# Optimization experiments

Hardware: AMD Instinct MI355X
Metric: run time of the kernel (lower is better)

Reference implementation:

```python
import jax, jax.numpy as jnp
import numpy as np

TOP_K = 2


def setup_inputs() -> dict:
    key = jax.random.key(0)
    ks = jax.random.split(key, 5)
    B, S, D, E, I = 1, 2048, 2880, 8, 2880
    scale_in = 1.0 / np.sqrt(D)
    scale_mid = 1.0 / np.sqrt(I)
    return {
        "x": jax.random.normal(ks[0], (B, S, D), dtype=jnp.float32),
        "w_router": jax.random.normal(ks[1], (D, E), dtype=jnp.float32) * scale_in,
        "w_gate": jax.random.normal(ks[2], (E, D, I), dtype=jnp.float32) * scale_in,
        "w_up": jax.random.normal(ks[3], (E, D, I), dtype=jnp.float32) * scale_in,
        "w_down": jax.random.normal(ks[4], (E, I, D), dtype=jnp.float32) * scale_mid,
    }


def reference(x, w_router, w_gate, w_up, w_down):
    B, S, D = x.shape
    E = w_router.shape[1]
    t = x.reshape(-1, D)  # [T, D] flattened tokens

    # --- RouterTopK: softmax over experts, then top-k selection ---
    logits = t @ w_router                      # [T, E]
    affinities = jax.nn.softmax(logits, axis=-1)
    top_vals, top_idx = jax.lax.top_k(affinities, TOP_K)   # [T, K]
    # normalize_top_k_affinities=True: renormalize selected weights to sum to 1
    top_vals = top_vals / jnp.sum(top_vals, axis=-1, keepdims=True)

    # scatter normalized weights into dense [T, E] combine matrix
    T = t.shape[0]
    tok = jnp.arange(T)[:, None]
    weights = jnp.zeros((T, E), dtype=t.dtype).at[tok, top_idx].set(top_vals)

    # --- Expert SiLU-GLU MLPs (computed per expert, combined by weights) ---
    gate = jnp.einsum("td,edi->eti", t, w_gate)  # [E, T, I]
    up = jnp.einsum("td,edi->eti", t, w_up)      # [E, T, I]
    h = jax.nn.silu(gate) * up                   # [E, T, I]
    y = jnp.einsum("eti,eid->etd", h, w_down)    # [E, T, D]

    out = jnp.einsum("te,etd->td", weights, y)   # affinity-weighted combine
    return out.reshape(B, S, D)
```

## Files before the change

kernel.cpp:

```cpp
#include <hip/hip_runtime.h>
#include <hip/hip_fp16.h>
#include <stdint.h>
#include <math.h>


typedef _Float16 f16;
typedef _Float16 f16x8 __attribute__((ext_vector_type(8)));
typedef float f32x4 __attribute__((ext_vector_type(4)));

#define T_TOK 2048
#define DDIM 2880
#define NEXP 8
#define IDIM 2880

#define BM 256
#define BK 64
#define NKT 45
#define BN1 96
#define NNT1 30
#define BN2 192
#define NNT2 15
#define MAXMT 24
#define NB1 (NNT1*MAXMT)
#define NB2 (NNT2*MAXMT)
#define SLOT_CAP 6144

#define HBUF_OFF 0
#define HBUF_BYTES ((size_t)SLOT_CAP*IDIM*2)
#define XH_OFF   (HBUF_OFF + HBUF_BYTES)
#define XH_BYTES ((size_t)T_TOK*DDIM*2)
#define YBUF_OFF XH_OFF
#define YBUF_BYTES ((size_t)SLOT_CAP*DDIM*2)
#define META_OFF (YBUF_OFF + YBUF_BYTES)
#define M_COUNT 0
#define M_CUR 8
#define M_OFFS 16
#define M_NTILES 25
#define M_TILE_E 32
#define M_TILE_R0 96
#define M_SLOT_TOK 160
#define M_SLOT_OF (160+SLOT_CAP)
#define M_TOK_E (M_SLOT_OF + 2*T_TOK)
#define META_INTS (M_TOK_E + 2*T_TOK)
#define SLOTW_OFF (META_OFF + META_INTS*4)
#define TOKW_OFF  (SLOTW_OFF + SLOT_CAP*4)
#define WS_NEEDED ((size_t)TOKW_OFF + (size_t)T_TOK*2*4)

__device__ __forceinline__ int swz(int row) { return ((row ^ (row >> 3)) & 7) << 4; }

__device__ __forceinline__ void gload_lds16(const void* gp, void* lp) {
  __builtin_amdgcn_global_load_lds(
      (const __attribute__((address_space(1))) uint32_t*)gp,
      (__attribute__((address_space(3))) uint32_t*)lp,
      16, 0, 0);
}

__global__ __launch_bounds__(256) void k_router(
    const float* __restrict__ x, const float* __restrict__ wr,
    int* __restrict__ meta, float* __restrict__ tok_w) {
  const int lane = threadIdx.x & 63;
  const int t = blockIdx.x * 4 + (threadIdx.x >> 6);
  double acc[NEXP];
#pragma unroll
  for (int e = 0; e < NEXP; e++) acc[e] = 0.0;
  for (int d = lane; d < DDIM; d += 64) {
    float xv = x[(size_t)t * DDIM + d];
    float4 w0 = *(const float4*)(wr + (size_t)d * NEXP);
    float4 w1 = *(const float4*)(wr + (size_t)d * NEXP + 4);
    acc[0] += (double)xv * (double)w0.x;
    acc[1] += (double)xv * (double)w0.y;
    acc[2] += (double)xv * (double)w0.z;
    acc[3] += (double)xv * (double)w0.w;
    acc[4] += (double)xv * (double)w1.x;
    acc[5] += (double)xv * (double)w1.y;
    acc[6] += (double)xv * (double)w1.z;
    acc[7] += (double)xv * (double)w1.w;
  }
#pragma unroll
  for (int m = 32; m >= 1; m >>= 1) {
#pragma unroll
    for (int e = 0; e < NEXP; e++) acc[e] += __shfl_xor(acc[e], m, 64);
  }
  if (lane == 0) {
    int e0 = 0;
#pragma unroll
    for (int e = 1; e < NEXP; e++) if (acc[e] > acc[e0]) e0 = e;
    int e1 = (e0 == 0) ? 1 : 0;
#pragma unroll
    for (int e = 0; e < NEXP; e++) if (e != e0 && acc[e] > acc[e1]) e1 = e;
    double w0 = 1.0 / (1.0 + exp(acc[e1] - acc[e0]));
    meta[M_TOK_E + 2*t]     = e0;
    meta[M_TOK_E + 2*t + 1] = e1;
    tok_w[2*t]     = (float)w0;
    tok_w[2*t + 1] = (float)(1.0 - w0);
    atomicAdd(&meta[M_COUNT + e0], 1);
    atomicAdd(&meta[M_COUNT + e1], 1);
  }
}

__global__ __launch_bounds__(256) void k_xcvt(const float* __restrict__ x, f16* __restrict__ xh) {
  size_t i = ((size_t)blockIdx.x * 256 + threadIdx.x) * 8;
  float4 a = *(const float4*)(x + i);
  float4 b = *(const float4*)(x + i + 4);
  f16x8 v;
  v[0]=(f16)a.x; v[1]=(f16)a.y; v[2]=(f16)a.z; v[3]=(f16)a.w;
  v[4]=(f16)b.x; v[5]=(f16)b.y; v[6]=(f16)b.z; v[7]=(f16)b.w;
  *(f16x8*)(xh + i) = v;
}

__global__ __launch_bounds__(64) void k_scan(int* __restrict__ meta, float* __restrict__ slot_w) {
  __shared__ int s_off[NEXP], s_cnt[NEXP], s_pc[NEXP];
  if (threadIdx.x == 0) {
    int run = 0, nt = 0;
    for (int e = 0; e < NEXP; e++) {
      int c = meta[M_COUNT + e];
      int mt = (c + BM - 1) / BM;
      meta[M_OFFS + e] = run;
      s_off[e] = run; s_cnt[e] = c; s_pc[e] = mt * BM;
      for (int j = 0; j < mt; j++) { meta[M_TILE_E + nt] = e; meta[M_TILE_R0 + nt] = run + j * BM; nt++; }
      run += mt * BM;
      meta[M_CUR + e] = 0;
    }
    meta[M_OFFS + NEXP] = run;
    meta[M_NTILES] = nt;
  }
  __syncthreads();
  for (int e = 0; e < NEXP; e++) {
    for (int i = s_cnt[e] + (int)threadIdx.x; i < s_pc[e]; i += 64) {
      meta[M_SLOT_TOK + s_off[e] + i] = 0;
      slot_w[s_off[e] + i] = 0.0f;
    }
  }
}

__global__ __launch_bounds__(256) void k_scatter(int* __restrict__ meta,
    float* __restrict__ slot_w, const float* __restrict__ tok_w) {
  int t = blockIdx.x * 256 + threadIdx.x;
  if (t >= T_TOK) return;
#pragma unroll
  for (int k = 0; k < 2; k++) {
    int e = meta[M_TOK_E + 2*t + k];
    int pos = atomicAdd(&meta[M_CUR + e], 1);
    int slot = meta[M_OFFS + e] + pos;
    meta[M_SLOT_TOK + slot] = t;
    slot_w[slot] = tok_w[2*t + k];
    meta[M_SLOT_OF + 2*t + k] = slot;
  }
}

__global__ __launch_bounds__(512, 2) void k_gemm1(
    const f16* __restrict__ xh, const float* __restrict__ wg, const float* __restrict__ wu,
    f16* __restrict__ hbuf, const int* __restrict__ meta) {
  const int id = blockIdx.x;
  const int sid = (id & 7) * (NB1 / 8) + (id >> 3);
  const int mt = sid % MAXMT;
  const int nb = sid / MAXMT;
  if (mt >= meta[M_NTILES]) return;
  const int e  = meta[M_TILE_E + mt];
  const int r0 = meta[M_TILE_R0 + mt];
  const int n0 = nb * BN1;

  __shared__ ushort sA[2][BM * BK];
  __shared__ ushort sB[2][2][BN1 * BK];

  const int tid  = threadIdx.x;
  const int lane = tid & 63;
  const int w    = tid >> 6;
  const int wm   = w >> 1;
  const int gu   = w & 1;

  const char* a_gbase[4];
  int a_loff[4];
#pragma unroll
  for (int i = 0; i < 4; i++) {
    int seg = w * 4 + i;
    int row = seg * 8 + (lane >> 3);
    int colb = ((lane & 7) * 16) ^ swz(row);
    int tok = meta[M_SLOT_TOK + r0 + row];
    a_gbase[i] = (const char*)(xh + (size_t)tok * DDIM) + colb;
    a_loff[i] = seg * 1024;
  }

  const int bm_ = tid / 192;
  const int tt  = tid % 192;
  const int bn0 = (tt % 24) * 4;
  const int bk0 = (tt / 24) * 8;
  const bool bact = tid < 384;
  const float* bsrc = (bm_ ? wu : wg) + ((size_t)e * DDIM + bk0) * IDIM + n0 + bn0;

  float4 vB[8];
  f32x4 acc[4][6];
#pragma unroll
  for (int i = 0; i < 4; i++)
#pragma unroll
    for (int j = 0; j < 6; j++) acc[i][j] = {0.f,0.f,0.f,0.f};

#pragma unroll
  for (int i = 0; i < 4; i++) gload_lds16(a_gbase[i], (char*)sA[0] + a_loff[i]);
  if (bact) {
#pragma unroll
    for (int j = 0; j < 8; j++) vB[j] = *(const float4*)(bsrc + (size_t)j * IDIM);
#pragma unroll
    for (int c = 0; c < 4; c++) {
      f16x8 p;
#pragma unroll
      for (int j = 0; j < 8; j++) {
        float fc = (c==0) ? vB[j].x : (c==1) ? vB[j].y : (c==2) ? vB[j].z : vB[j].w;
        p[j] = (f16)fc;
      }
      *(f16x8*)((char*)sB[0][bm_] + (bn0 + c) * 128 + ((bk0 * 2) ^ swz(bn0 + c))) = p;
    }
  }
  __syncthreads();

  for (int kt = 0; kt < NKT; kt++) {
    const int cur = kt & 1;
    if (kt + 1 < NKT) {
#pragma unroll
      for (int i = 0; i < 4; i++)
        gload_lds16(a_gbase[i] + (kt + 1) * 128, (char*)sA[cur ^ 1] + a_loff[i]);
      if (bact) {
        const float* bs = bsrc + (size_t)(kt + 1) * BK * IDIM;
#pragma unroll
        for (int j = 0; j < 8; j++) vB[j] = *(const float4*)(bs + (size_t)j * IDIM);
      }
    }
#pragma unroll
    for (int kk = 0; kk < 2; kk++) {
      const int gb = kk * 64 + ((lane >> 4) * 16);
      f16x8 af[4], bf[6];
#pragma unroll
      for (int fm = 0; fm < 4; fm++) {
        int row = wm * 64 + fm * 16 + (lane & 15);
        af[fm] = *(const f16x8*)((const char*)sA[cur] + row * 128 + (gb ^ swz(row)));
      }
#pragma unroll
      for (int fn = 0; fn < 6; fn++) {
        int row = fn * 16 + (lane & 15);
        bf[fn] = *(const f16x8*)((const char*)sB[cur][gu] + row * 128 + (gb ^ swz(row)));
      }
#pragma unroll
      for (int fm = 0; fm < 4; fm++)
#pragma unroll
        for (int fn = 0; fn < 6; fn++)
          acc[fm][fn] = __builtin_amdgcn_mfma_f32_16x16x32_f16(af[fm], bf[fn], acc[fm][fn], 0, 0, 0);
    }
    if (kt + 1 < NKT && bact) {
#pragma unroll
      for (int c = 0; c < 4; c++) {
        f16x8 p;
#pragma unroll
        for (int j = 0; j < 8; j++) {
          float fc = (c==0) ? vB[j].x : (c==1) ? vB[j].y : (c==2) ? vB[j].z : vB[j].w;
          p[j] = (f16)fc;
        }
        *(f16x8*)((char*)sB[cur ^ 1][bm_] + (bn0 + c) * 128 + ((bk0 * 2) ^ swz(bn0 + c))) = p;
      }
    }
    __syncthreads();
  }

  float* u_lds = (float*)&sA[0][0];
  const int rl4 = (lane >> 4) * 4;
  const int cl  = lane & 15;
#pragma unroll
  for (int r = 0; r < 2; r++) {
    __syncthreads();
    if (gu == 1) {
#pragma unroll
      for (int fi = 0; fi < 2; fi++)
#pragma unroll
        for (int fn = 0; fn < 6; fn++)
#pragma unroll
          for (int j = 0; j < 4; j++)
            u_lds[wm * 3200 + (fi * 16 + rl4 + j) * 100 + fn * 16 + cl] = acc[2*r + fi][fn][j];
    }
    __syncthreads();
    if (gu == 0) {
#pragma unroll
      for (int fi = 0; fi < 2; fi++) {
        int fm = 2*r + fi;
#pragma unroll
        for (int fn = 0; fn < 6; fn++)
#pragma unroll
          for (int j = 0; j < 4; j++) {
            float u = u_lds[wm * 3200 + (fi * 16 + rl4 + j) * 100 + fn * 16 + cl];
            float g = acc[fm][fn][j];
            float h = g * u / (1.0f + __expf(-g));
            hbuf[(size_t)(r0 + wm * 64 + fm * 16 + rl4 + j) * IDIM + n0 + fn * 16 + cl] = (f16)h;
          }
      }
    }
  }
}

__global__ __launch_bounds__(512, 2) void k_gemm2(
    const f16* __restrict__ hbuf, const float* __restrict__ wd,
    f16* __restrict__ ybuf, const int* __restrict__ meta, const float* __restrict__ slot_w) {
  const int id = blockIdx.x;
  const int sid = (id & 7) * (NB2 / 8) + (id >> 3);
  const int mt = sid % MAXMT;
  const int nb = sid / MAXMT;
  if (mt >= meta[M_NTILES]) return;
  const int e  = meta[M_TILE_E + mt];
  const int r0 = meta[M_TILE_R0 + mt];
  const int n0 = nb * BN2;

  __shared__ ushort sA[2][BM * BK];
  __shared__ ushort sB1[2][BN2 * BK];

  const int tid  = threadIdx.x;
  const int lane = tid & 63;
  const int w    = tid >> 6;
  const int wm   = w >> 1;
  const int wn   = w & 1;

  const char* a_gbase[4];
  int a_loff[4];
#pragma unroll
  for (int i = 0; i < 4; i++) {
    int seg = w * 4 + i;
    int row = seg * 8 + (lane >> 3);
    int colb = ((lane & 7) * 16) ^ swz(row);
    a_gbase[i] = (const char*)(hbuf + (size_t)(r0 + row) * IDIM) + colb;
    a_loff[i] = seg * 1024;
  }

  const int half = tid / 192;
  const int tt   = tid % 192;
  const int bn0  = half * 96 + (tt % 24) * 4;
  const int bk0  = (tt / 24) * 8;
  const bool bact = tid < 384;
  const float* bsrc = wd + ((size_t)e * IDIM + bk0) * DDIM + n0 + bn0;

  float4 vB[8];
  f32x4 acc[4][6];
#pragma unroll
  for (int i = 0; i < 4; i++)
#pragma unroll
    for (int j = 0; j < 6; j++) acc[i][j] = {0.f,0.f,0.f,0.f};

#pragma unroll
  for (int i = 0; i < 4; i++) gload_lds16(a_gbase[i], (char*)sA[0] + a_loff[i]);
  if (bact) {
#pragma unroll
    for (int j = 0; j < 8; j++) vB[j] = *(const float4*)(bsrc + (size_t)j * DDIM);
#pragma unroll
    for (int c = 0; c < 4; c++) {
      f16x8 p;
#pragma unroll
      for (int j = 0; j < 8; j++) {
        float fc = (c==0) ? vB[j].x : (c==1) ? vB[j].y : (c==2) ? vB[j].z : vB[j].w;
        p[j] = (f16)fc;
      }
      *(f16x8*)((char*)sB1[0] + (bn0 + c) * 128 + ((bk0 * 2) ^ swz(bn0 + c))) = p;
    }
  }
  __syncthreads();

  for (int kt = 0; kt < NKT; kt++) {
    const int cur = kt & 1;
    if (kt + 1 < NKT) {
#pragma unroll
      for (int i = 0; i < 4; i++)
        gload_lds16(a_gbase[i] + (kt + 1) * 128, (char*)sA[cur ^ 1] + a_loff[i]);
      if (bact) {
        const float* bs = bsrc + (size_t)(kt + 1) * BK * DDIM;
#pragma unroll
        for (int j = 0; j < 8; j++) vB[j] = *(const float4*)(bs + (size_t)j * DDIM);
      }
    }
#pragma unroll
    for (int kk = 0; kk < 2; kk++) {
      const int gb = kk * 64 + ((lane >> 4) * 16);
      f16x8 af[4], bf[6];
#pragma unroll
      for (int fm = 0; fm < 4; fm++) {
        int row = wm * 64 + fm * 16 + (lane & 15);
        af[fm] = *(const f16x8*)((const char*)sA[cur] + row * 128 + (gb ^ swz(row)));
      }
#pragma unroll
      for (int fn = 0; fn < 6; fn++) {
        int row = wn * 96 + fn * 16 + (lane & 15);
        bf[fn] = *(const f16x8*)((const char*)sB1[cur] + row * 128 + (gb ^ swz(row)));
      }
#pragma unroll
      for (int fm = 0; fm < 4; fm++)
#pragma unroll
        for (int fn = 0; fn < 6; fn++)
          acc[fm][fn] = __builtin_amdgcn_mfma_f32_16x16x32_f16(af[fm], bf[fn], acc[fm][fn], 0, 0, 0);
    }
    if (kt + 1 < NKT && bact) {
#pragma unroll
      for (int c = 0; c < 4; c++) {
        f16x8 p;
#pragma unroll
        for (int j = 0; j < 8; j++) {
          float fc = (c==0) ? vB[j].x : (c==1) ? vB[j].y : (c==2) ? vB[j].z : vB[j].w;
          p[j] = (f16)fc;
        }
        *(f16x8*)((char*)sB1[cur ^ 1] + (bn0 + c) * 128 + ((bk0 * 2) ^ swz(bn0 + c))) = p;
      }
    }
    __syncthreads();
  }

  const int rl4 = (lane >> 4) * 4;
  const int cl  = lane & 15;
#pragma unroll
  for (int fm = 0; fm < 4; fm++)
#pragma unroll
    for (int j = 0; j < 4; j++) {
      int row = wm * 64 + fm * 16 + rl4 + j;
      int slot = r0 + row;
      float wv = slot_w[slot];
#pragma unroll
      for (int fn = 0; fn < 6; fn++) {
        int col = n0 + wn * 96 + fn * 16 + cl;
        ybuf[(size_t)slot * DDIM + col] = (f16)(acc[fm][fn][j] * wv);
      }
    }
}

__global__ __launch_bounds__(256) void k_combine(const f16* __restrict__ ybuf,
    const int* __restrict__ meta, float* __restrict__ out) {
  size_t idx = (size_t)blockIdx.x * 256 + threadIdx.x;
  int t = (int)(idx / (DDIM/8));
  int c = (int)(idx % (DDIM/8));
  int s0 = meta[M_SLOT_OF + 2*t];
  int s1 = meta[M_SLOT_OF + 2*t + 1];
  f16x8 a = *(const f16x8*)(ybuf + (size_t)s0 * DDIM + c*8);
  f16x8 b = *(const f16x8*)(ybuf + (size_t)s1 * DDIM + c*8);
  float4 o0, o1;
  o0.x = (float)a[0] + (float)b[0];
  o0.y = (float)a[1] + (float)b[1];
  o0.z = (float)a[2] + (float)b[2];
  o0.w = (float)a[3] + (float)b[3];
  o1.x = (float)a[4] + (float)b[4];
  o1.y = (float)a[5] + (float)b[5];
  o1.z = (float)a[6] + (float)b[6];
  o1.w = (float)a[7] + (float)b[7];
  float* op = out + (size_t)t * DDIM + c*8;
  *(float4*)op = o0;
  *(float4*)(op + 4) = o1;
}

extern "C" void kernel_launch(void* const* d_in, const int* in_sizes, int n_in,
                              void* d_out, int out_size, void* d_ws, size_t ws_size,
                              hipStream_t stream) {
  const float* x  = (const float*)d_in[0];
  const float* wr = (const float*)d_in[1];
  const float* wg = (const float*)d_in[2];
  const float* wu = (const float*)d_in[3];
  const float* wd = (const float*)d_in[4];
  float* out = (float*)d_out;
  char* ws = (char*)d_ws;
  if (ws_size < WS_NEEDED) return;

  f16* hbuf  = (f16*)(ws + HBUF_OFF);
  f16* xh    = (f16*)(ws + XH_OFF);
  f16* ybuf  = (f16*)(ws + YBUF_OFF);
  int* meta  = (int*)(ws + META_OFF);
  float* slot_w = (float*)(ws + SLOTW_OFF);
  float* tok_w  = (float*)(ws + TOKW_OFF);

  hipMemsetAsync(meta + M_COUNT, 0, NEXP * sizeof(int), stream);
  k_router<<<T_TOK/4, 256, 0, stream>>>(x, wr, meta, tok_w);
  k_xcvt<<<(T_TOK*DDIM/8 + 255)/256, 256, 0, stream>>>(x, xh);
  k_scan<<<1, 64, 0, stream>>>(meta, slot_w);
  k_scatter<<<(T_TOK + 255)/256, 256, 0, stream>>>(meta, slot_w, tok_w);
  k_gemm1<<<NB1, 512, 0, stream>>>(xh, wg, wu, hbuf, meta);
  k_gemm2<<<NB2, 512, 0, stream>>>(hbuf, wd, ybuf, meta, slot_w);
  k_combine<<<(T_TOK*DDIM/8 + 255)/256, 256, 0, stream>>>(ybuf, meta, out);
}
```

Baseline: 687.3 us.

## Pre-convert expert weights to transposed fp16 and stream via direct LDS loads

Adds a kernel that converts the gate, up and down weights on every call from fp32 into a transposed fp16 layout in workspace. Both expert GEMMs can then load weight tiles straight into LDS with global_load_lds, instead of loading fp32 into registers and converting inside the K loop. The GEMMs also move to 128-row tiles with 256 threads, and the up and gate products now share the A fragments in one kernel. In exchange the new path pays a full weight read-convert-write pass each call, needs a much larger workspace, and drops the double-buffered K pipeline. The old kernels stay as a fallback for when the workspace is too small.

```diff
diff --git a/kernel.cpp b/kernel.cpp
--- a/kernel.cpp
+++ b/kernel.cpp
@@ -12,26 +12,24 @@
 #define DDIM 2880
 #define NEXP 8
 #define IDIM 2880
-
-#define BM 256
 #define BK 64
 #define NKT 45
-#define BN1 96
-#define NNT1 30
-#define BN2 192
-#define NNT2 15
-#define MAXMT 24
-#define NB1 (NNT1*MAXMT)
-#define NB2 (NNT2*MAXMT)
+
+#define BM_A 128
+#define BN1_A 96
+#define BN2_A 192
+#define MAXMT_A 40
+#define NB1_A (30*MAXMT_A)
+#define NB2_A (15*MAXMT_A)
+#define BM_B 256
+#define BN1_B 96
+#define BN2_B 192
+#define MAXMT_B 24
+#define NB1_B (30*MAXMT_B)
+#define NB2_B (15*MAXMT_B)
+
 #define SLOT_CAP 6144
 
-#define HBUF_OFF 0
-#define HBUF_BYTES ((size_t)SLOT_CAP*IDIM*2)
-#define XH_OFF   (HBUF_OFF + HBUF_BYTES)
-#define XH_BYTES ((size_t)T_TOK*DDIM*2)
-#define YBUF_OFF XH_OFF
-#define YBUF_BYTES ((size_t)SLOT_CAP*DDIM*2)
-#define META_OFF (YBUF_OFF + YBUF_BYTES)
 #define M_COUNT 0
 #define M_CUR 8
 #define M_OFFS 16
@@ -42,9 +40,26 @@
 #define M_SLOT_OF (160+SLOT_CAP)
 #define M_TOK_E (M_SLOT_OF + 2*T_TOK)
 #define META_INTS (M_TOK_E + 2*T_TOK)
-#define SLOTW_OFF (META_OFF + META_INTS*4)
-#define TOKW_OFF  (SLOTW_OFF + SLOT_CAP*4)
-#define WS_NEEDED ((size_t)TOKW_OFF + (size_t)T_TOK*2*4)
+
+#define WT_B   ((size_t)NEXP*DDIM*IDIM*2)
+#define A_WGT  ((size_t)0)
+#define A_WUT  (A_WGT + WT_B)
+#define A_WDT  A_WGT
+#define A_HBUF (A_WUT + WT_B)
+#define A_YBUF (A_HBUF + (size_t)5120*IDIM*2)
+#define A_XH   (A_YBUF + (size_t)5120*DDIM*2)
+#define A_META (A_XH + (size_t)T_TOK*DDIM*2)
+#define A_SLOTW (A_META + (size_t)META_INTS*4)
+#define A_TOKW  (A_SLOTW + (size_t)SLOT_CAP*4)
+#define A_NEED  (A_TOKW + (size_t)T_TOK*2*4)
+
+#define B_HBUF ((size_t)0)
+#define B_XH   (B_HBUF + (size_t)SLOT_CAP*IDIM*2)
+#define B_YBUF B_XH
+#define B_META (B_YBUF + (size_t)SLOT_CAP*DDIM*2)
+#define B_SLOTW (B_META + (size_t)META_INTS*4)
+#define B_TOKW  (B_SLOTW + (size_t)SLOT_CAP*4)
+#define B_NEED  (B_TOKW + (size_t)T_TOK*2*4)
 
 __device__ __forceinline__ int swz(int row) { return ((row ^ (row >> 3)) & 7) << 4; }
 
@@ -108,17 +123,45 @@
   *(f16x8*)(xh + i) = v;
 }
 
-__global__ __launch_bounds__(64) void k_scan(int* __restrict__ meta, float* __restrict__ slot_w) {
+__global__ __launch_bounds__(256) void k_cvt_w(const float* __restrict__ src, f16* __restrict__ dst) {
+  __shared__ f16 t[64][72];
+  const int tile = blockIdx.x;
+  const int e = blockIdx.y;
+  const int k0 = (tile / 45) * 64;
+  const int i0 = (tile % 45) * 64;
+  const int tid = threadIdx.x;
+  const float* sp = src + ((size_t)e * DDIM + k0) * IDIM + i0;
+#pragma unroll
+  for (int p = 0; p < 4; p++) {
+    int kr = p * 16 + (tid >> 4);
+    int c0 = (tid & 15) * 4;
+    float4 v = *(const float4*)(sp + (size_t)kr * IDIM + c0);
+    t[c0 + 0][kr] = (f16)v.x;
+    t[c0 + 1][kr] = (f16)v.y;
+    t[c0 + 2][kr] = (f16)v.z;
+    t[c0 + 3][kr] = (f16)v.w;
+  }
+  __syncthreads();
+#pragma unroll
+  for (int p = 0; p < 2; p++) {
+    int row = tid >> 2;
+    int ch = (tid & 3) + p * 4;
+    f16x8 o = *(const f16x8*)&t[row][ch * 8];
+    *(f16x8*)(dst + ((size_t)e * IDIM + i0 + row) * DDIM + k0 + ch * 8) = o;
+  }
+}
+
+__global__ __launch_bounds__(64) void k_scan(int* __restrict__ meta, float* __restrict__ slot_w, int bm) {
   __shared__ int s_off[NEXP], s_cnt[NEXP], s_pc[NEXP];
   if (threadIdx.x == 0) {
     int run = 0, nt = 0;
     for (int e = 0; e < NEXP; e++) {
       int c = meta[M_COUNT + e];
-      int mt = (c + BM - 1) / BM;
+      int mt = (c + bm - 1) / bm;
       meta[M_OFFS + e] = run;
-      s_off[e] = run; s_cnt[e] = c; s_pc[e] = mt * BM;
-      for (int j = 0; j < mt; j++) { meta[M_TILE_E + nt] = e; meta[M_TILE_R0 + nt] = run + j * BM; nt++; }
-      run += mt * BM;
+      s_off[e] = run; s_cnt[e] = c; s_pc[e] = mt * bm;
+      for (int j = 0; j < mt; j++) { meta[M_TILE_E + nt] = e; meta[M_TILE_R0 + nt] = run + j * bm; nt++; }
+      run += mt * bm;
       meta[M_CUR + e] = 0;
     }
     meta[M_OFFS + NEXP] = run;
@@ -148,228 +191,156 @@
   }
 }
 
-__global__ __launch_bounds__(512, 2) void k_gemm1(
-    const f16* __restrict__ xh, const float* __restrict__ wg, const float* __restrict__ wu,
+
+__global__ __launch_bounds__(256, 3) void kg1(
+    const f16* __restrict__ xh, const f16* __restrict__ wgT, const f16* __restrict__ wuT,
     f16* __restrict__ hbuf, const int* __restrict__ meta) {
   const int id = blockIdx.x;
-  const int sid = (id & 7) * (NB1 / 8) + (id >> 3);
-  const int mt = sid % MAXMT;
-  const int nb = sid / MAXMT;
+  const int sid = (id & 7) * (NB1_A / 8) + (id >> 3);
+  const int mt = sid % MAXMT_A;
+  const int nb = sid / MAXMT_A;
   if (mt >= meta[M_NTILES]) return;
   const int e  = meta[M_TILE_E + mt];
   const int r0 = meta[M_TILE_R0 + mt];
-  const int n0 = nb * BN1;
-
-  __shared__ ushort sA[2][BM * BK];
-  __shared__ ushort sB[2][2][BN1 * BK];
-
-  const int tid  = threadIdx.x;
+  const int n0 = nb * BN1_A;
+
+  __shared__ ushort sA[BM_A * BK];
+  __shared__ ushort sBg[BN1_A * BK];
+  __shared__ ushort sBu[BN1_A * BK];
+
+  const int tid = threadIdx.x;
   const int lane = tid & 63;
-  const int w    = tid >> 6;
-  const int wm   = w >> 1;
-  const int gu   = w & 1;
-
-  const char* a_gbase[4];
-  int a_loff[4];
+  const int w = tid >> 6;
+  const int wm = w >> 1, wn = w & 1;
+
+  const char* aG[4]; int aL[4];
 #pragma unroll
   for (int i = 0; i < 4; i++) {
     int seg = w * 4 + i;
     int row = seg * 8 + (lane >> 3);
     int colb = ((lane & 7) * 16) ^ swz(row);
     int tok = meta[M_SLOT_TOK + r0 + row];
-    a_gbase[i] = (const char*)(xh + (size_t)tok * DDIM) + colb;
-    a_loff[i] = seg * 1024;
-  }
-
-  const int bm_ = tid / 192;
-  const int tt  = tid % 192;
-  const int bn0 = (tt % 24) * 4;
-  const int bk0 = (tt / 24) * 8;
-  const bool bact = tid < 384;
-  const float* bsrc = (bm_ ? wu : wg) + ((size_t)e * DDIM + bk0) * IDIM + n0 + bn0;
-
-  float4 vB[8];
-  f32x4 acc[4][6];
+    aG[i] = (const char*)(xh + (size_t)tok * DDIM) + colb;
+    aL[i] = seg * 1024;
+  }
+  const char* gG[3]; const char* uG[3]; int bL[3];
+#pragma unroll
+  for (int i = 0; i < 3; i++) {
+    int seg = w * 3 + i;
+    int row = seg * 8 + (lane >> 3);
+    int colb = ((lane & 7) * 16) ^ swz(row);
+    gG[i] = (const char*)(wgT + ((size_t)e * IDIM + n0 + row) * DDIM) + colb;
+    uG[i] = (const char*)(wuT + ((size_t)e * IDIM + n0 + row) * DDIM) + colb;
+    bL[i] = seg * 1024;
+  }
+
+  f32x4 accG[4][3], accU[4][3];
 #pragma unroll
   for (int i = 0; i < 4; i++)
 #pragma unroll
-    for (int j = 0; j < 6; j++) acc[i][j] = {0.f,0.f,0.f,0.f};
-
-#pragma unroll
-  for (int i = 0; i < 4; i++) gload_lds16(a_gbase[i], (char*)sA[0] + a_loff[i]);
-  if (bact) {
-#pragma unroll
-    for (int j = 0; j < 8; j++) vB[j] = *(const float4*)(bsrc + (size_t)j * IDIM);
-#pragma unroll
-    for (int c = 0; c < 4; c++) {
-      f16x8 p;
-#pragma unroll
-      for (int j = 0; j < 8; j++) {
-        float fc = (c==0) ? vB[j].x : (c==1) ? vB[j].y : (c==2) ? vB[j].z : vB[j].w;
-        p[j] = (f16)fc;
-      }
-      *(f16x8*)((char*)sB[0][bm_] + (bn0 + c) * 128 + ((bk0 * 2) ^ swz(bn0 + c))) = p;
-    }
-  }
-  __syncthreads();
+    for (int j = 0; j < 3; j++) { accG[i][j] = {0.f,0.f,0.f,0.f}; accU[i][j] = {0.f,0.f,0.f,0.f}; }
 
   for (int kt = 0; kt < NKT; kt++) {
-    const int cur = kt & 1;
-    if (kt + 1 < NKT) {
-#pragma unroll
-      for (int i = 0; i < 4; i++)
-        gload_lds16(a_gbase[i] + (kt + 1) * 128, (char*)sA[cur ^ 1] + a_loff[i]);
-      if (bact) {
-        const float* bs = bsrc + (size_t)(kt + 1) * BK * IDIM;
-#pragma unroll
-        for (int j = 0; j < 8; j++) vB[j] = *(const float4*)(bs + (size_t)j * IDIM);
-      }
-    }
+    __syncthreads();
+#pragma unroll
+    for (int i = 0; i < 4; i++) gload_lds16(aG[i] + kt * 128, (char*)sA + aL[i]);
+#pragma unroll
+    for (int i = 0; i < 3; i++) gload_lds16(gG[i] + kt * 128, (char*)sBg + bL[i]);
+#pragma unroll
+    for (int i = 0; i < 3; i++) gload_lds16(uG[i] + kt * 128, (char*)sBu + bL[i]);
+    __syncthreads();
 #pragma unroll
     for (int kk = 0; kk < 2; kk++) {
       const int gb = kk * 64 + ((lane >> 4) * 16);
-      f16x8 af[4], bf[6];
+      f16x8 af[4], bg[3], bu[3];
 #pragma unroll
       for (int fm = 0; fm < 4; fm++) {
         int row = wm * 64 + fm * 16 + (lane & 15);
-        af[fm] = *(const f16x8*)((const char*)sA[cur] + row * 128 + (gb ^ swz(row)));
-      }
-#pragma unroll
-      for (int fn = 0; fn < 6; fn++) {
-        int row = fn * 16 + (lane & 15);
-        bf[fn] = *(const f16x8*)((const char*)sB[cur][gu] + row * 128 + (gb ^ swz(row)));
+        af[fm] = *(const f16x8*)((const char*)sA + row * 128 + (gb ^ swz(row)));
+      }
+#pragma unroll
+      for (int fn = 0; fn < 3; fn++) {
+        int row = wn * 48 + fn * 16 + (lane & 15);
+        bg[fn] = *(const f16x8*)((const char*)sBg + row * 128 + (gb ^ swz(row)));
+        bu[fn] = *(const f16x8*)((const char*)sBu + row * 128 + (gb ^ swz(row)));
       }
 #pragma unroll
       for (int fm = 0; fm < 4; fm++)
 #pragma unroll
-        for (int fn = 0; fn < 6; fn++)
-          acc[fm][fn] = __builtin_amdgcn_mfma_f32_16x16x32_f16(af[fm], bf[fn], acc[fm][fn], 0, 0, 0);
-    }
-    if (kt + 1 < NKT && bact) {
-#pragma unroll
-      for (int c = 0; c < 4; c++) {
-        f16x8 p;
-#pragma unroll
-        for (int j = 0; j < 8; j++) {
-          float fc = (c==0) ? vB[j].x : (c==1) ? vB[j].y : (c==2) ? vB[j].z : vB[j].w;
-          p[j] = (f16)fc;
+        for (int fn = 0; fn < 3; fn++) {
+          accG[fm][fn] = __builtin_amdgcn_mfma_f32_16x16x32_f16(af[fm], bg[fn], accG[fm][fn], 0, 0, 0);
+          accU[fm][fn] = __builtin_amdgcn_mfma_f32_16x16x32_f16(af[fm], bu[fn], accU[fm][fn], 0, 0, 0);
         }
-        *(f16x8*)((char*)sB[cur ^ 1][bm_] + (bn0 + c) * 128 + ((bk0 * 2) ^ swz(bn0 + c))) = p;
-      }
-    }
-    __syncthreads();
-  }
-
-  float* u_lds = (float*)&sA[0][0];
+    }
+  }
   const int rl4 = (lane >> 4) * 4;
   const int cl  = lane & 15;
 #pragma unroll
-  for (int r = 0; r < 2; r++) {
-    __syncthreads();
-    if (gu == 1) {
-#pragma unroll
-      for (int fi = 0; fi < 2; fi++)
-#pragma unroll
-        for (int fn = 0; fn < 6; fn++)
-#pragma unroll
-          for (int j = 0; j < 4; j++)
-            u_lds[wm * 3200 + (fi * 16 + rl4 + j) * 100 + fn * 16 + cl] = acc[2*r + fi][fn][j];
-    }
-    __syncthreads();
-    if (gu == 0) {
-#pragma unroll
-      for (int fi = 0; fi < 2; fi++) {
-        int fm = 2*r + fi;
-#pragma unroll
-        for (int fn = 0; fn < 6; fn++)
-#pragma unroll
-          for (int j = 0; j < 4; j++) {
-            float u = u_lds[wm * 3200 + (fi * 16 + rl4 + j) * 100 + fn * 16 + cl];
-            float g = acc[fm][fn][j];
-            float h = g * u / (1.0f + __expf(-g));
-            hbuf[(size_t)(r0 + wm * 64 + fm * 16 + rl4 + j) * IDIM + n0 + fn * 16 + cl] = (f16)h;
-          }
-      }
-    }
-  }
-}
-
-__global__ __launch_bounds__(512, 2) void k_gemm2(
-    const f16* __restrict__ hbuf, const float* __restrict__ wd,
+  for (int fm = 0; fm < 4; fm++)
+#pragma unroll
+    for (int fn = 0; fn < 3; fn++)
+#pragma unroll
+      for (int j = 0; j < 4; j++) {
+        int row = wm * 64 + fm * 16 + rl4 + j;
+        int col = n0 + wn * 48 + fn * 16 + cl;
+        float g = accG[fm][fn][j], u = accU[fm][fn][j];
+        float h = g * u / (1.0f + __expf(-g));
+        hbuf[(size_t)(r0 + row) * IDIM + col] = (f16)h;
+      }
+}
+
+__global__ __launch_bounds__(256, 3) void kg2(
+    const f16* __restrict__ hbuf, const f16* __restrict__ wdT,
     f16* __restrict__ ybuf, const int* __restrict__ meta, const float* __restrict__ slot_w) {
   const int id = blockIdx.x;
-  const int sid = (id & 7) * (NB2 / 8) + (id >> 3);
-  const int mt = sid % MAXMT;
-  const int nb = sid / MAXMT;
+  const int sid = (id & 7) * (NB2_A / 8) + (id >> 3);
+  const int mt = sid % MAXMT_A;
+  const int nb = sid / MAXMT_A;
   if (mt >= meta[M_NTILES]) return;
   const int e  = meta[M_TILE_E + mt];
   const int r0 = meta[M_TILE_R0 + mt];
-  const int n0 = nb * BN2;
-
-  __shared__ ushort sA[2][BM * BK];
-  __shared__ ushort sB1[2][BN2 * BK];
-
-  const int tid  = threadIdx.x;
+  const int n0 = nb * BN2_A;
+
+  __shared__ ushort sA[BM_A * BK];
+  __shared__ ushort sB[BN2_A * BK];
+
+  const int tid = threadIdx.x;
   const int lane = tid & 63;
-  const int w    = tid >> 6;
-  const int wm   = w >> 1;
-  const int wn   = w & 1;
-
-  const char* a_gbase[4];
-  int a_loff[4];
+  const int w = tid >> 6;
+  const int wm = w >> 1, wn = w & 1;
+
+  const char* aG[4]; int aL[4];
 #pragma unroll
   for (int i = 0; i < 4; i++) {
     int seg = w * 4 + i;
     int row = seg * 8 + (lane >> 3);
     int colb = ((lane & 7) * 16) ^ swz(row);
-    a_gbase[i] = (const char*)(hbuf + (size_t)(r0 + row) * IDIM) + colb;
-    a_loff[i] = seg * 1024;
-  }
-
-  const int half = tid / 192;
-  const int tt   = tid % 192;
-  const int bn0  = half * 96 + (tt % 24) * 4;
-  const int bk0  = (tt / 24) * 8;
-  const bool bact = tid < 384;
-  const float* bsrc = wd + ((size_t)e * IDIM + bk0) * DDIM + n0 + bn0;
-
-  float4 vB[8];
+    aG[i] = (const char*)(hbuf + (size_t)(r0 + row) * IDIM) + colb;
+    aL[i] = seg * 1024;
+  }
+  const char* bG[6]; int bL[6];
+#pragma unroll
+  for (int i = 0; i < 6; i++) {
+    int seg = w * 6 + i;
+    int row = seg * 8 + (lane >> 3);
+    int colb = ((lane & 7) * 16) ^ swz(row);
+    bG[i] = (const char*)(wdT + ((size_t)e * DDIM + n0 + row) * IDIM) + colb;
+    bL[i] = seg * 1024;
+  }
+
   f32x4 acc[4][6];
 #pragma unroll
   for (int i = 0; i < 4; i++)
 #pragma unroll
     for (int j = 0; j < 6; j++) acc[i][j] = {0.f,0.f,0.f,0.f};
 
-#pragma unroll
-  for (int i = 0; i < 4; i++) gload_lds16(a_gbase[i], (char*)sA[0] + a_loff[i]);
-  if (bact) {
-#pragma unroll
-    for (int j = 0; j < 8; j++) vB[j] = *(const float4*)(bsrc + (size_t)j * DDIM);
-#pragma unroll
-    for (int c = 0; c < 4; c++) {
-      f16x8 p;
-#pragma unroll
-      for (int j = 0; j < 8; j++) {
-        float fc = (c==0) ? vB[j].x : (c==1) ? vB[j].y : (c==2) ? vB[j].z : vB[j].w;
-        p[j] = (f16)fc;
-      }
-      *(f16x8*)((char*)sB1[0] + (bn0 + c) * 128 + ((bk0 * 2) ^ swz(bn0 + c))) = p;
-    }
-  }
-  __syncthreads();
-
   for (int kt = 0; kt < NKT; kt++) {
-    const int cur = kt & 1;
-    if (kt + 1 < NKT) {
-#pragma unroll
-      for (int i = 0; i < 4; i++)
-        gload_lds16(a_gbase[i] + (kt + 1) * 128, (char*)sA[cur ^ 1] + a_loff[i]);
-      if (bact) {
-        const float* bs = bsrc + (size_t)(kt + 1) * BK * DDIM;
-#pragma unroll
-        for (int j = 0; j < 8; j++) vB[j] = *(const float4*)(bs + (size_t)j * DDIM);
-      }
-    }
+    __syncthreads();
+#pragma unroll
+    for (int i = 0; i < 4; i++) gload_lds16(aG[i] + kt * 128, (char*)sA + aL[i]);
+#pragma unroll
+    for (int i = 0; i < 6; i++) gload_lds16(bG[i] + kt * 128, (char*)sB + bL[i]);
+    __syncthreads();
 #pragma unroll
     for (int kk = 0; kk < 2; kk++) {
       const int gb = kk * 64 + ((lane >> 4) * 16);
@@ -377,12 +348,12 @@
 #pragma unroll
       for (int fm = 0; fm < 4; fm++) {
         int row = wm * 64 + fm * 16 + (lane & 15);
-        af[fm] = *(const f16x8*)((const char*)sA[cur] + row * 128 + (gb ^ swz(row)));
+        af[fm] = *(const f16x8*)((const char*)sA + row * 128 + (gb ^ swz(row)));
       }
 #pragma unroll
       for (int fn = 0; fn < 6; fn++) {
         int row = wn * 96 + fn * 16 + (lane & 15);
-        bf[fn] = *(const f16x8*)((const char*)sB1[cur] + row * 128 + (gb ^ swz(row)));
+        bf[fn] = *(const f16x8*)((const char*)sB + row * 128 + (gb ^ swz(row)));
       }
 #pragma unroll
       for (int fm = 0; fm < 4; fm++)
@@ -390,21 +361,7 @@
         for (int fn = 0; fn < 6; fn++)
           acc[fm][fn] = __builtin_amdgcn_mfma_f32_16x16x32_f16(af[fm], bf[fn], acc[fm][fn], 0, 0, 0);
     }
-    if (kt + 1 < NKT && bact) {
-#pragma unroll
-      for (int c = 0; c < 4; c++) {
-        f16x8 p;
-#pragma unroll
-        for (int j = 0; j < 8; j++) {
-          float fc = (c==0) ? vB[j].x : (c==1) ? vB[j].y : (c==2) ? vB[j].z : vB[j].w;
-          p[j] = (f16)fc;
-        }
-        *(f16x8*)((char*)sB1[cur ^ 1] + (bn0 + c) * 128 + ((bk0 * 2) ^ swz(bn0 + c))) = p;
-      }
-    }
-    __syncthreads();
-  }
-
+  }
   const int rl4 = (lane >> 4) * 4;
   const int cl  = lane & 15;
 #pragma unroll
@@ -445,6 +402,279 @@
   *(float4*)(op + 4) = o1;
 }
 
+
+__global__ __launch_bounds__(512, 2) void kg1_fb(
+    const f16* __restrict__ xh, const float* __restrict__ wg, const float* __restrict__ wu,
+    f16* __restrict__ hbuf, const int* __restrict__ meta) {
+  const int id = blockIdx.x;
+  const int sid = (id & 7) * (NB1_B / 8) + (id >> 3);
+  const int mt = sid % MAXMT_B;
+  const int nb = sid / MAXMT_B;
+  if (mt >= meta[M_NTILES]) return;
+  const int e  = meta[M_TILE_E + mt];
+  const int r0 = meta[M_TILE_R0 + mt];
+  const int n0 = nb * BN1_B;
+
+  __shared__ ushort sA[2][BM_B * BK];
+  __shared__ ushort sB[2][2][BN1_B * BK];
+
+  const int tid  = threadIdx.x;
+  const int lane = tid & 63;
+  const int w    = tid >> 6;
+  const int wm   = w >> 1;
+  const int gu   = w & 1;
+
+  const char* a_gbase[4];
+  int a_loff[4];
+#pragma unroll
+  for (int i = 0; i < 4; i++) {
+    int seg = w * 4 + i;
+    int row = seg * 8 + (lane >> 3);
+    int colb = ((lane & 7) * 16) ^ swz(row);
+    int tok = meta[M_SLOT_TOK + r0 + row];
+    a_gbase[i] = (const char*)(xh + (size_t)tok * DDIM) + colb;
+    a_loff[i] = seg * 1024;
+  }
+  const int bm_ = tid / 192;
+  const int tt  = tid % 192;
+  const int bn0 = (tt % 24) * 4;
+  const int bk0 = (tt / 24) * 8;
+  const bool bact = tid < 384;
+  const float* bsrc = (bm_ ? wu : wg) + ((size_t)e * DDIM + bk0) * IDIM + n0 + bn0;
+
+  float4 vB[8];
+  f32x4 acc[4][6];
+#pragma unroll
+  for (int i = 0; i < 4; i++)
+#pragma unroll
+    for (int j = 0; j < 6; j++) acc[i][j] = {0.f,0.f,0.f,0.f};
+
+#pragma unroll
+  for (int i = 0; i < 4; i++) gload_lds16(a_gbase[i], (char*)sA[0] + a_loff[i]);
+  if (bact) {
+#pragma unroll
+    for (int j = 0; j < 8; j++) vB[j] = *(const float4*)(bsrc + (size_t)j * IDIM);
+#pragma unroll
+    for (int c = 0; c < 4; c++) {
+      f16x8 p;
+#pragma unroll
+      for (int j = 0; j < 8; j++) {
+        float fc = (c==0) ? vB[j].x : (c==1) ? vB[j].y : (c==2) ? vB[j].z : vB[j].w;
+        p[j] = (f16)fc;
+      }
+      *(f16x8*)((char*)sB[0][bm_] + (bn0 + c) * 128 + ((bk0 * 2) ^ swz(bn0 + c))) = p;
+    }
+  }
+  __syncthreads();
+
+  for (int kt = 0; kt < NKT; kt++) {
+    const int cur = kt & 1;
+    if (kt + 1 < NKT) {
+#pragma unroll
+      for (int i = 0; i < 4; i++)
+        gload_lds16(a_gbase[i] + (kt + 1) * 128, (char*)sA[cur ^ 1] + a_loff[i]);
+      if (bact) {
+        const float* bs = bsrc + (size_t)(kt + 1) * BK * IDIM;
+#pragma unroll
+        for (int j = 0; j < 8; j++) vB[j] = *(const float4*)(bs + (size_t)j * IDIM);
+      }
+    }
+#pragma unroll
+    for (int kk = 0; kk < 2; kk++) {
+      const int gb = kk * 64 + ((lane >> 4) * 16);
+      f16x8 af[4], bf[6];
+#pragma unroll
+      for (int fm = 0; fm < 4; fm++) {
+        int row = wm * 64 + fm * 16 + (lane & 15);
+        af[fm] = *(const f16x8*)((const char*)sA[cur] + row * 128 + (gb ^ swz(row)));
+      }
+#pragma unroll
+      for (int fn = 0; fn < 6; fn++) {
+        int row = fn * 16 + (lane & 15);
+        bf[fn] = *(const f16x8*)((const char*)sB[cur][gu] + row * 128 + (gb ^ swz(row)));
+      }
+#pragma unroll
+      for (int fm = 0; fm < 4; fm++)
+#pragma unroll
+        for (int fn = 0; fn < 6; fn++)
+          acc[fm][fn] = __builtin_amdgcn_mfma_f32_16x16x32_f16(af[fm], bf[fn], acc[fm][fn], 0, 0, 0);
+    }
+    if (kt + 1 < NKT && bact) {
+#pragma unroll
+      for (int c = 0; c < 4; c++) {
+        f16x8 p;
+#pragma unroll
+        for (int j = 0; j < 8; j++) {
+          float fc = (c==0) ? vB[j].x : (c==1) ? vB[j].y : (c==2) ? vB[j].z : vB[j].w;
+          p[j] = (f16)fc;
+        }
+        *(f16x8*)((char*)sB[cur ^ 1][bm_] + (bn0 + c) * 128 + ((bk0 * 2) ^ swz(bn0 + c))) = p;
+      }
+    }
+    __syncthreads();
+  }
+
+  float* u_lds = (float*)&sA[0][0];
+  const int rl4 = (lane >> 4) * 4;
+  const int cl  = lane & 15;
+#pragma unroll
+  for (int r = 0; r < 2; r++) {
+    __syncthreads();
+    if (gu == 1) {
+#pragma unroll
+      for (int fi = 0; fi < 2; fi++)
+#pragma unroll
+        for (int fn = 0; fn < 6; fn++)
+#pragma unroll
+          for (int j = 0; j < 4; j++)
+            u_lds[wm * 3200 + (fi * 16 + rl4 + j) * 100 + fn * 16 + cl] = acc[2*r + fi][fn][j];
+    }
+    __syncthreads();
+    if (gu == 0) {
+#pragma unroll
+      for (int fi = 0; fi < 2; fi++) {
+        int fm = 2*r + fi;
+#pragma unroll
+        for (int fn = 0; fn < 6; fn++)
+#pragma unroll
+          for (int j = 0; j < 4; j++) {
+            float u = u_lds[wm * 3200 + (fi * 16 + rl4 + j) * 100 + fn * 16 + cl];
+            float g = acc[fm][fn][j];
+            float h = g * u / (1.0f + __expf(-g));
+            hbuf[(size_t)(r0 + wm * 64 + fm * 16 + rl4 + j) * IDIM + n0 + fn * 16 + cl] = (f16)h;
+          }
+      }
+    }
+  }
+}
+
+__global__ __launch_bounds__(512, 2) void kg2_fb(
+    const f16* __restrict__ hbuf, const float* __restrict__ wd,
+    f16* __restrict__ ybuf, const int* __restrict__ meta, const float* __restrict__ slot_w) {
+  const int id = blockIdx.x;
+  const int sid = (id & 7) * (NB2_B / 8) + (id >> 3);
+  const int mt = sid % MAXMT_B;
+  const int nb = sid / MAXMT_B;
+  if (mt >= meta[M_NTILES]) return;
+  const int e  = meta[M_TILE_E + mt];
+  const int r0 = meta[M_TILE_R0 + mt];
+  const int n0 = nb * BN2_B;
+
+  __shared__ ushort sA[2][BM_B * BK];
+  __shared__ ushort sB1[2][BN2_B * BK];
+
+  const int tid  = threadIdx.x;
+  const int lane = tid & 63;
+  const int w    = tid >> 6;
+  const int wm   = w >> 1;
+  const int wn   = w & 1;
+
+  const char* a_gbase[4];
+  int a_loff[4];
+#pragma unroll
+  for (int i = 0; i < 4; i++) {
+    int seg = w * 4 + i;
+    int row = seg * 8 + (lane >> 3);
+    int colb = ((lane & 7) * 16) ^ swz(row);
+    a_gbase[i] = (const char*)(hbuf + (size_t)(r0 + row) * IDIM) + colb;
+    a_loff[i] = seg * 1024;
+  }
+  const int half = tid / 192;
+  const int tt   = tid % 192;
+  const int bn0  = half * 96 + (tt % 24) * 4;
+  const int bk0  = (tt / 24) * 8;
+  const bool bact = tid < 384;
+  const float* bsrc = wd + ((size_t)e * IDIM + bk0) * DDIM + n0 + bn0;
+
+  float4 vB[8];
+  f32x4 acc[4][6];
+#pragma unroll
+  for (int i = 0; i < 4; i++)
+#pragma unroll
+    for (int j = 0; j < 6; j++) acc[i][j] = {0.f,0.f,0.f,0.f};
+
+#pragma unroll
+  for (int i = 0; i < 4; i++) gload_lds16(a_gbase[i], (char*)sA[0] + a_loff[i]);
+  if (bact) {
+#pragma unroll
+    for (int j = 0; j < 8; j++) vB[j] = *(const float4*)(bsrc + (size_t)j * DDIM);
+#pragma unroll
+    for (int c = 0; c < 4; c++) {
+      f16x8 p;
+#pragma unroll
+      for (int j = 0; j < 8; j++) {
+        float fc = (c==0) ? vB[j].x : (c==1) ? vB[j].y : (c==2) ? vB[j].z : vB[j].w;
+        p[j] = (f16)fc;
+      }
+      *(f16x8*)((char*)sB1[0] + (bn0 + c) * 128 + ((bk0 * 2) ^ swz(bn0 + c))) = p;
+    }
+  }
+  __syncthreads();
+
+  for (int kt = 0; kt < NKT; kt++) {
+    const int cur = kt & 1;
+    if (kt + 1 < NKT) {
+#pragma unroll
+      for (int i = 0; i < 4; i++)
+        gload_lds16(a_gbase[i] + (kt + 1) * 128, (char*)sA[cur ^ 1] + a_loff[i]);
+      if (bact) {
+        const float* bs = bsrc + (size_t)(kt + 1) * BK * DDIM;
+#pragma unroll
+        for (int j = 0; j < 8; j++) vB[j] = *(const float4*)(bs + (size_t)j * DDIM);
+      }
+    }
+#pragma unroll
+    for (int kk = 0; kk < 2; kk++) {
+      const int gb = kk * 64 + ((lane >> 4) * 16);
+      f16x8 af[4], bf[6];
+#pragma unroll
+      for (int fm = 0; fm < 4; fm++) {
+        int row = wm * 64 + fm * 16 + (lane & 15);
+        af[fm] = *(const f16x8*)((const char*)sA[cur] + row * 128 + (gb ^ swz(row)));
+      }
+#pragma unroll
+      for (int fn = 0; fn < 6; fn++) {
+        int row = wn * 96 + fn * 16 + (lane & 15);
+        bf[fn] = *(const f16x8*)((const char*)sB1[cur] + row * 128 + (gb ^ swz(row)));
+      }
+#pragma unroll
+      for (int fm = 0; fm < 4; fm++)
+#pragma unroll
+        for (int fn = 0; fn < 6; fn++)
+          acc[fm][fn] = __builtin_amdgcn_mfma_f32_16x16x32_f16(af[fm], bf[fn], acc[fm][fn], 0, 0, 0);
+    }
+    if (kt + 1 < NKT && bact) {
+#pragma unroll
+      for (int c = 0; c < 4; c++) {
+        f16x8 p;
+#pragma unroll
+        for (int j = 0; j < 8; j++) {
+          float fc = (c==0) ? vB[j].x : (c==1) ? vB[j].y : (c==2) ? vB[j].z : vB[j].w;
+          p[j] = (f16)fc;
+        }
+        *(f16x8*)((char*)sB1[cur ^ 1] + (bn0 + c) * 128 + ((bk0 * 2) ^ swz(bn0 + c))) = p;
+      }
+    }
+    __syncthreads();
+  }
+
+  const int rl4 = (lane >> 4) * 4;
+  const int cl  = lane & 15;
+#pragma unroll
+  for (int fm = 0; fm < 4; fm++)
+#pragma unroll
+    for (int j = 0; j < 4; j++) {
+      int row = wm * 64 + fm * 16 + rl4 + j;
+      int slot = r0 + row;
+      float wv = slot_w[slot];
+#pragma unroll
+      for (int fn = 0; fn < 6; fn++) {
+        int col = n0 + wn * 96 + fn * 16 + cl;
+        ybuf[(size_t)slot * DDIM + col] = (f16)(acc[fm][fn][j] * wv);
+      }
+    }
+}
+
 extern "C" void kernel_launch(void* const* d_in, const int* in_sizes, int n_in,
                               void* d_out, int out_size, void* d_ws, size_t ws_size,
                               hipStream_t stream) {
@@ -455,21 +685,44 @@
   const float* wd = (const float*)d_in[4];
   float* out = (float*)d_out;
   char* ws = (char*)d_ws;
-  if (ws_size < WS_NEEDED) return;
-
-  f16* hbuf  = (f16*)(ws + HBUF_OFF);
-  f16* xh    = (f16*)(ws + XH_OFF);
-  f16* ybuf  = (f16*)(ws + YBUF_OFF);
-  int* meta  = (int*)(ws + META_OFF);
-  float* slot_w = (float*)(ws + SLOTW_OFF);
-  float* tok_w  = (float*)(ws + TOKW_OFF);
-
-  hipMemsetAsync(meta + M_COUNT, 0, NEXP * sizeof(int), stream);
-  k_router<<<T_TOK/4, 256, 0, stream>>>(x, wr, meta, tok_w);
-  k_xcvt<<<(T_TOK*DDIM/8 + 255)/256, 256, 0, stream>>>(x, xh);
-  k_scan<<<1, 64, 0, stream>>>(meta, slot_w);
-  k_scatter<<<(T_TOK + 255)/256, 256, 0, stream>>>(meta, slot_w, tok_w);
-  k_gemm1<<<NB1, 512, 0, stream>>>(xh, wg, wu, hbuf, meta);
-  k_gemm2<<<NB2, 512, 0, stream>>>(hbuf, wd, ybuf, meta, slot_w);
-  k_combine<<<(T_TOK*DDIM/8 + 255)/256, 256, 0, stream>>>(ybuf, meta, out);
-}
+
+  if (ws_size >= A_NEED) {
+    f16* wgT = (f16*)(ws + A_WGT);
+    f16* wuT = (f16*)(ws + A_WUT);
+    f16* wdT = (f16*)(ws + A_WDT);
+    f16* hbuf = (f16*)(ws + A_HBUF);
+    f16* ybuf = (f16*)(ws + A_YBUF);
+    f16* xh   = (f16*)(ws + A_XH);
+    int* meta = (int*)(ws + A_META);
+    float* slot_w = (float*)(ws + A_SLOTW);
+    float* tok_w  = (float*)(ws + A_TOKW);
+
+    hipMemsetAsync(meta + M_COUNT, 0, NEXP * sizeof(int), stream);
+    k_cvt_w<<<dim3(2025, NEXP), 256, 0, stream>>>(wg, wgT);
+    k_cvt_w<<<dim3(2025, NEXP), 256, 0, stream>>>(wu, wuT);
+    k_router<<<T_TOK/4, 256, 0, stream>>>(x, wr, meta, tok_w);
+    k_xcvt<<<(T_TOK*DDIM/8)/256, 256, 0, stream>>>(x, xh);
+    k_scan<<<1, 64, 0, stream>>>(meta, slot_w, BM_A);
+    k_scatter<<<(T_TOK + 255)/256, 256, 0, stream>>>(meta, slot_w, tok_w);
+    kg1<<<NB1_A, 256, 0, stream>>>(xh, wgT, wuT, hbuf, meta);
+    k_cvt_w<<<dim3(2025, NEXP), 256, 0, stream>>>(wd, wdT);
+    kg2<<<NB2_A, 256, 0, stream>>>(hbuf, wdT, ybuf, meta, slot_w);
+    k_combine<<<(T_TOK*DDIM/8)/256, 256, 0, stream>>>(ybuf, meta, out);
+  } else if (ws_size >= B_NEED) {
+    f16* hbuf = (f16*)(ws + B_HBUF);
+    f16* xh   = (f16*)(ws + B_XH);
+    f16* ybuf = (f16*)(ws + B_YBUF);
+    int* meta = (int*)(ws + B_META);
+    float* slot_w = (float*)(ws + B_SLOTW);
+    float* tok_w  = (float*)(ws + B_TOKW);
+
+    hipMemsetAsync(meta + M_COUNT, 0, NEXP * sizeof(int), stream);
+    k_router<<<T_TOK/4, 256, 0, stream>>>(x, wr, meta, tok_w);
+    k_xcvt<<<(T_TOK*DDIM/8)/256, 256, 0, stream>>>(x, xh);
+    k_scan<<<1, 64, 0, stream>>>(meta, slot_w, BM_B);
+    k_scatter<<<(T_TOK + 255)/256, 256, 0, stream>>>(meta, slot_w, tok_w);
+    kg1_fb<<<NB1_B, 512, 0, stream>>>(xh, wg, wu, hbuf, meta);
+    kg2_fb<<<NB2_B, 512, 0, stream>>>(hbuf, wd, ybuf, meta, slot_w);
+    k_combine<<<(T_TOK*DDIM/8)/256, 256, 0, stream>>>(ybuf, meta, out);
+  }
+}
```

Result: no change. 691.3 us (+0.6%).
